# Performance work log

Hardware: AMD Instinct MI355X
Metric: run time of the kernel (lower is better)

## Reference

```python
import jax, jax.numpy as jnp
import numpy as np

N_NODES = 100000
N_EDGES = 3200000
NFEAT, NHID, OPFEAT = 128, 128, 64
EPS = 1e-06


def setup_inputs() -> dict:
    key = jax.random.key(0)
    ks = jax.random.split(key, 20)
    def u(k, shape, s):
        return jax.random.uniform(k, shape, jnp.float32, -s, s)
    inp = {
        'x': jax.random.normal(ks[0], (N_NODES, NFEAT), jnp.float32),
        'edge_rows': jax.random.randint(ks[1], (N_EDGES,), 0, N_NODES, jnp.int32),
        'edge_cols': jax.random.randint(ks[2], (N_EDGES,), 0, N_NODES, jnp.int32),
        'edge_vals': jax.random.uniform(ks[3], (N_EDGES,), jnp.float32),
        # fc layers (torch Linear: weight [out, in])
        'fc1_w': u(ks[4], (NHID, NFEAT), 1.0 / np.sqrt(NFEAT)),
        'fc1_b': u(ks[5], (NHID,), 1.0 / np.sqrt(NFEAT)),
        'fc2_w': u(ks[6], (NHID, NHID), 1.0 / np.sqrt(NHID)),
        'fc2_b': u(ks[7], (NHID,), 1.0 / np.sqrt(NHID)),
        'ln_gamma': jnp.ones((NHID,), jnp.float32),
        'ln_beta': jnp.zeros((NHID,), jnp.float32),
    }
    s = 1.0 / np.sqrt(NHID)
    for i, out_f in zip(range(1, 5), [NHID, NHID, NHID, OPFEAT]):
        k1, k2, k3 = jax.random.split(jax.random.fold_in(key, 100 + i), 3)
        inp[f'gc{i}_wn'] = u(k1, (NHID, out_f), s)
        inp[f'gc{i}_ws'] = u(k2, (NHID, out_f), s)
        inp[f'gc{i}_b'] = u(k3, (out_f,), s)
    return inp


def _gcn_first_order(x, wn, ws, b, rows, cols, vals):
    # act_self + sparse_adj @ (x @ wn) + bias
    act_self = x @ ws                      # [N, out]
    support = x @ wn                       # [N, out]
    gathered = support[cols] * vals[:, None]   # [E, out] irregular gather
    act_neighbor = jax.ops.segment_sum(gathered, rows, num_segments=x.shape[0])
    return act_self + act_neighbor + b


def _layer_norm(x, gamma, beta):
    mean = jnp.mean(x, axis=-1, keepdims=True)
    std = jnp.std(x, axis=-1, keepdims=True, ddof=1)  # torch .std is unbiased
    return gamma * (x - mean) / (std + EPS) + beta


def reference(x, edge_rows, edge_cols, edge_vals,
              fc1_w, fc1_b, fc2_w, fc2_b, ln_gamma, ln_beta,
              gc1_wn, gc1_ws, gc1_b, gc2_wn, gc2_ws, gc2_b,
              gc3_wn, gc3_ws, gc3_b, gc4_wn, gc4_ws, gc4_b):
    h = jax.nn.relu(x @ fc1_w.T + fc1_b)
    h = jax.nn.relu(h @ fc2_w.T + fc2_b)
    h = _layer_norm(h, ln_gamma, ln_beta)
    h = jax.nn.relu(_gcn_first_order(h, gc1_wn, gc1_ws, gc1_b, edge_rows, edge_cols, edge_vals))
    h = jax.nn.relu(_gcn_first_order(h, gc2_wn, gc2_ws, gc2_b, edge_rows, edge_cols, edge_vals))
    h = jax.nn.relu(_gcn_first_order(h, gc3_wn, gc3_ws, gc3_b, edge_rows, edge_cols, edge_vals))
    h = jax.nn.relu(_gcn_first_order(h, gc4_wn, gc4_ws, gc4_b, edge_rows, edge_cols, edge_vals))
    return h
```

## Files before the change

### kernel.cpp

```cpp
#include <hip/hip_runtime.h>

constexpr int N_NODES = 100000;
constexpr int N_EDGES = 3200000;
constexpr float EPS = 1e-6f;

constexpr int NBKT = 196;
constexpr int BKT_SHIFT = 9;
constexpr int BKT_ROWS = 512;
constexpr int ARENA_STRIDE = 18432;
constexpr int EPB1 = 8000;
constexpr int NBLK1 = 400;
constexpr int CAP = 72;

typedef __attribute__((ext_vector_type(8))) short bfrag;
typedef __attribute__((ext_vector_type(4))) float ffrag;

__device__ __forceinline__ unsigned short f2bf(float f) {
    unsigned int u = __float_as_uint(f);
    u += 0x7FFFu + ((u >> 16) & 1u);
    return (unsigned short)(u >> 16);
}
__device__ __forceinline__ float bf_lo(unsigned int w) { return __uint_as_float(w << 16); }
__device__ __forceinline__ float bf_hi(unsigned int w) { return __uint_as_float(w & 0xFFFF0000u); }

__global__ __launch_bounds__(256) void prep_w_k(
    const float* __restrict__ fc1_w, const float* __restrict__ fc2_w,
    const float* __restrict__ wn0, const float* __restrict__ ws0,
    const float* __restrict__ wn1, const float* __restrict__ ws1,
    const float* __restrict__ wn2, const float* __restrict__ ws2,
    const float* __restrict__ wn3, const float* __restrict__ ws3,
    unsigned short* __restrict__ Wb)
{
    int idx = blockIdx.x * 256 + threadIdx.x;
    if (idx >= 147456) return;
    float v;
    if (idx < 32768) {
        int r = idx >> 7, k = idx & 127;
        v = (r < 128) ? fc1_w[r * 128 + k] : fc2_w[(r - 128) * 128 + k];
    } else if (idx < 131072) {
        int idx2 = idx - 32768;
        int l = idx2 >> 15, w = idx2 & 32767;
        int o = w >> 8, k = w & 255;
        const float* wn = l == 0 ? wn0 : l == 1 ? wn1 : wn2;
        const float* ws = l == 0 ? ws0 : l == 1 ? ws1 : ws2;
        v = (k < 128) ? ws[k * 128 + o] : wn[(k - 128) * 128 + o];
    } else {
        int idx3 = idx - 131072;
        int o = idx3 >> 7, k = idx3 & 127;
        v = (o < 64) ? wn3[k * 64 + o] : ws3[k * 64 + (o - 64)];
    }
    Wb[idx] = f2bf(v);
}

template<int MODE, bool A_FP32>
__global__ __launch_bounds__(256, 2) void mfma_gemm_k(
    const void* Av, const unsigned short* __restrict__ Wg_,
    const float* __restrict__ bias,
    const float* __restrict__ gamma, const float* __restrict__ beta,
    unsigned short* __restrict__ Yb, float* Tout)
{
    constexpr int NT = 8;
    __shared__ unsigned short Bs[128 * 136];
    const int tid = threadIdx.x;

    const uint4* Wg = (const uint4*)Wg_;
    uint4* Bs4 = (uint4*)Bs;
    for (int i = tid; i < 128 * 16; i += 256) {
        int n = i >> 4, c = i & 15;
        Bs4[n * 17 + c] = Wg[i];
    }

    const int wave = tid >> 6, lane = tid & 63;
    const int quad = lane >> 4, l16 = lane & 15;
    const long base = (long)blockIdx.x * 128 + wave * 32;

    union AU { uint4 q; bfrag v; unsigned short s[8]; };
    bfrag a[2][4];
#pragma unroll
    for (int mt = 0; mt < 2; mt++) {
        long node = base + mt * 16 + l16;
        bool ok = node < N_NODES;
        if (A_FP32) {
            const float4* Ar = (const float4*)((const float*)Av + node * 128);
#pragma unroll
            for (int t = 0; t < 4; t++) {
                AU u;
                if (ok) {
                    float4 f0 = Ar[t * 8 + quad * 2];
                    float4 f1 = Ar[t * 8 + quad * 2 + 1];
                    u.s[0] = f2bf(f0.x); u.s[1] = f2bf(f0.y);
                    u.s[2] = f2bf(f0.z); u.s[3] = f2bf(f0.w);
                    u.s[4] = f2bf(f1.x); u.s[5] = f2bf(f1.y);
                    u.s[6] = f2bf(f1.z); u.s[7] = f2bf(f1.w);
                } else u.q = make_uint4(0, 0, 0, 0);
                a[mt][t] = u.v;
            }
        } else {
            const uint4* Ar = (const uint4*)((const unsigned short*)Av + node * 128);
#pragma unroll
            for (int t = 0; t < 4; t++) {
                AU u;
                u.q = ok ? Ar[t * 4 + quad] : make_uint4(0, 0, 0, 0);
                a[mt][t] = u.v;
            }
        }
    }
    __syncthreads();

    ffrag acc[2][NT];
#pragma unroll
    for (int mt = 0; mt < 2; mt++)
#pragma unroll
        for (int nt = 0; nt < NT; nt++) acc[mt][nt] = (ffrag)0.f;

#pragma unroll
    for (int t = 0; t < 4; t++)
#pragma unroll
        for (int nt = 0; nt < NT; nt++) {
            bfrag b = *(const bfrag*)&Bs[(nt * 16 + l16) * 136 + t * 32 + quad * 8];
            acc[0][nt] = __builtin_amdgcn_mfma_f32_16x16x32_bf16(a[0][t], b, acc[0][nt], 0, 0, 0);
            acc[1][nt] = __builtin_amdgcn_mfma_f32_16x16x32_bf16(a[1][t], b, acc[1][nt], 0, 0, 0);
        }

    if (MODE == 0) {
        float bv[NT];
#pragma unroll
        for (int nt = 0; nt < NT; nt++) bv[nt] = bias[nt * 16 + l16];
#pragma unroll
        for (int mt = 0; mt < 2; mt++)
#pragma unroll
            for (int reg = 0; reg < 4; reg++) {
                long node = base + mt * 16 + quad * 4 + reg;
                if (node >= N_NODES) continue;
#pragma unroll
                for (int nt = 0; nt < NT; nt++)
                    Yb[node * 128 + nt * 16 + l16] = f2bf(fmaxf(acc[mt][nt][reg] + bv[nt], 0.f));
            }
    } else if (MODE == 1) {
        float bv[NT], gv[NT], bev[NT];
#pragma unroll
        for (int nt = 0; nt < NT; nt++) {
            bv[nt] = bias[nt * 16 + l16];
            gv[nt] = gamma[nt * 16 + l16];
            bev[nt] = beta[nt * 16 + l16];
        }
#pragma unroll
        for (int mt = 0; mt < 2; mt++)
#pragma unroll
            for (int reg = 0; reg < 4; reg++) {
                long node = base + mt * 16 + quad * 4 + reg;
                if (node >= N_NODES) continue;
                float v[NT], s = 0.f, sq = 0.f;
#pragma unroll
                for (int nt = 0; nt < NT; nt++) {
                    v[nt] = fmaxf(acc[mt][nt][reg] + bv[nt], 0.f);
                    s += v[nt]; sq += v[nt] * v[nt];
                }
#pragma unroll
                for (int off = 1; off < 16; off <<= 1) {
                    s  += __shfl_xor(s, off, 64);
                    sq += __shfl_xor(sq, off, 64);
                }
                float mean = s * (1.f / 128.f);
                float var = fmaxf((sq - 128.f * mean * mean) * (1.f / 127.f), 0.f);
                float inv = 1.f / (sqrtf(var) + EPS);
#pragma unroll
                for (int nt = 0; nt < NT; nt++)
                    Yb[node * 128 + nt * 16 + l16] = f2bf(gv[nt] * (v[nt] - mean) * inv + bev[nt]);
            }
    } else {
        float bv[4];
#pragma unroll
        for (int i = 0; i < 4; i++) bv[i] = bias[i * 16 + l16];
#pragma unroll
        for (int mt = 0; mt < 2; mt++)
#pragma unroll
            for (int reg = 0; reg < 4; reg++) {
                long node = base + mt * 16 + quad * 4 + reg;
                if (node >= N_NODES) continue;
#pragma unroll
                for (int nt = 0; nt < 4; nt++)
                    Yb[node * 64 + nt * 16 + l16] = f2bf(acc[mt][nt][reg]);
#pragma unroll
                for (int nt = 4; nt < 8; nt++)
                    Tout[node * 64 + (nt - 4) * 16 + l16] = acc[mt][nt][reg] + bv[nt - 4];
            }
    }
}

__global__ __launch_bounds__(256, 2) void fused_gemm_k(
    const unsigned short* __restrict__ A1, const unsigned short* __restrict__ A2,
    const unsigned short* __restrict__ Wg_, const float* __restrict__ bias,
    unsigned short* __restrict__ Y)
{
    constexpr int NT = 8;
    __shared__ unsigned short Bs[128 * 264];
    const int tid = threadIdx.x;

    const uint4* Wg = (const uint4*)Wg_;
    uint4* Bs4 = (uint4*)Bs;
    for (int i = tid; i < 128 * 32; i += 256) {
        int n = i >> 5, c = i & 31;
        Bs4[n * 33 + c] = Wg[i];
    }

    const int wave = tid >> 6, lane = tid & 63;
    const int quad = lane >> 4, l16 = lane & 15;
    const long base = (long)blockIdx.x * 128 + wave * 32;

    union AU { uint4 q; bfrag v; };
    bfrag a[2][8];
#pragma unroll
    for (int mt = 0; mt < 2; mt++) {
        long node = base + mt * 16 + l16;
        bool ok = node < N_NODES;
        const uint4* A1r = (const uint4*)(A1 + node * 128);
        const uint4* A2r = (const uint4*)(A2 + node * 128);
#pragma unroll
        for (int t = 0; t < 4; t++) {
            AU u1, u2;
            u1.q = ok ? A1r[t * 4 + quad] : make_uint4(0, 0, 0, 0);
            u2.q = ok ? A2r[t * 4 + quad] : make_uint4(0, 0, 0, 0);
            a[mt][t] = u1.v;
            a[mt][4 + t] = u2.v;
        }
    }
    __syncthreads();

    ffrag acc[2][NT];
#pragma unroll
    for (int mt = 0; mt < 2; mt++)
#pragma unroll
        for (int nt = 0; nt < NT; nt++) acc[mt][nt] = (ffrag)0.f;

#pragma unroll
    for (int t = 0; t < 8; t++)
#pragma unroll
        for (int nt = 0; nt < NT; nt++) {
            bfrag b = *(const bfrag*)&Bs[(nt * 16 + l16) * 264 + t * 32 + quad * 8];
            acc[0][nt] = __builtin_amdgcn_mfma_f32_16x16x32_bf16(a[0][t], b, acc[0][nt], 0, 0, 0);
            acc[1][nt] = __builtin_amdgcn_mfma_f32_16x16x32_bf16(a[1][t], b, acc[1][nt], 0, 0, 0);
        }

    float bv[NT];
#pragma unroll
    for (int nt = 0; nt < NT; nt++) bv[nt] = bias[nt * 16 + l16];
#pragma unroll
    for (int mt = 0; mt < 2; mt++)
#pragma unroll
        for (int reg = 0; reg < 4; reg++) {
            long node = base + mt * 16 + quad * 4 + reg;
            if (node >= N_NODES) continue;
#pragma unroll
            for (int nt = 0; nt < NT; nt++)
                Y[node * 128 + nt * 16 + l16] = f2bf(fmaxf(acc[mt][nt][reg] + bv[nt], 0.f));
        }
}

__global__ __launch_bounds__(256) void bin_k(
    const int* __restrict__ rows, const int* __restrict__ cols,
    const float* __restrict__ vals, int* gcur,
    unsigned* __restrict__ arena_e, unsigned short* __restrict__ arena_r)
{
    __shared__ int hist[NBKT];
    __shared__ int lstart[NBKT];
    __shared__ int lcur[NBKT];
    __shared__ int gbase[NBKT];
    __shared__ unsigned st_e[EPB1];
    __shared__ unsigned short st_r[EPB1];
    __shared__ unsigned char st_b[EPB1];
    const int tid = threadIdx.x;
    const int e0 = blockIdx.x * EPB1;
    const int ecnt = min(EPB1, N_EDGES - e0);

    for (int i = tid; i < NBKT; i += 256) hist[i] = 0;
    __syncthreads();
    for (int i = tid; i < ecnt; i += 256)
        atomicAdd(&hist[rows[e0 + i] >> BKT_SHIFT], 1);
    __syncthreads();
    if (tid == 0) {
        int s = 0;
        for (int b = 0; b < NBKT; b++) { lstart[b] = s; s += hist[b]; }
    }
    __syncthreads();
    for (int i = tid; i < NBKT; i += 256) lcur[i] = lstart[i];
    __syncthreads();
    for (int i = tid; i < ecnt; i += 256) {
        int r = rows[e0 + i];
        int b = r >> BKT_SHIFT;
        unsigned entry = ((unsigned)cols[e0 + i] << 15)
                       | (unsigned)(f2bf(vals[e0 + i]) & 0x7FFF);
        int pos = atomicAdd(&lcur[b], 1);
        st_e[pos] = entry;
        st_r[pos] = (unsigned short)(r & (BKT_ROWS - 1));
        st_b[pos] = (unsigned char)b;
    }
    __syncthreads();
    for (int b = tid; b < NBKT; b += 256) {
        int cnt = lcur[b] - lstart[b];
        gbase[b] = cnt > 0 ? atomicAdd(&gcur[b], cnt) : 0;
    }
    __syncthreads();
    for (int i = tid; i < ecnt; i += 256) {
        int b = st_b[i];
        int off = gbase[b] + (i - lstart[b]);
        if (off < ARENA_STRIDE) {
            long dest = (long)b * ARENA_STRIDE + off;
            arena_e[dest] = st_e[i];
            arena_r[dest] = st_r[i];
        }
    }
}

__global__ __launch_bounds__(1024) void build_k(
    const int* __restrict__ gcur, const unsigned* __restrict__ arena_e,
    const unsigned short* __restrict__ arena_r,
    unsigned* __restrict__ csr, int* __restrict__ cursor)
{
    __shared__ int cnt[BKT_ROWS];
    const int tid = threadIdx.x;
    const int b = blockIdx.x;
    for (int i = tid; i < BKT_ROWS; i += 1024) cnt[i] = 0;
    __syncthreads();
    const int ec = min(gcur[b], ARENA_STRIDE);
    const long abase = (long)b * ARENA_STRIDE;
    for (int i = tid; i < ec; i += 1024) {
        unsigned entry = arena_e[abase + i];
        int rib = arena_r[abase + i] & (BKT_ROWS - 1);
        int rank = atomicAdd(&cnt[rib], 1);
        if (rank < CAP)
            csr[((long)b * BKT_ROWS + rib) * CAP + rank] = entry;
    }
    __syncthreads();
    for (int i = tid; i < BKT_ROWS; i += 1024) {
        int gr = b * BKT_ROWS + i;
        if (gr < N_NODES) cursor[gr] = min(cnt[i], CAP);
    }
}

__global__ __launch_bounds__(256) void gather_k(
    const int* __restrict__ cursor, const unsigned* __restrict__ csr,
    const unsigned short* __restrict__ Sb, unsigned short* __restrict__ G)
{
    int node = blockIdx.x * 4 + (threadIdx.x >> 6);
    if (node >= N_NODES) return;
    int lane = threadIdx.x & 63;
    int fl = lane & 15, ep = lane >> 4;
    const long s = (long)node * CAP;
    const int total = min(cursor[node], CAP);

    float acc[8] = {0, 0, 0, 0, 0, 0, 0, 0};
    const uint4* S4 = (const uint4*)Sb;

    for (int base = 0; base < total; base += 64) {
        int idx = base + lane;
        unsigned ed = (idx < total) ? csr[s + idx] : 0u;
        int cnt = total - base; if (cnt > 64) cnt = 64;
        int U = cnt >> 4;
        int j = ep;
        for (int u = 0; u < U; u++, j += 16) {
            unsigned p0 = (unsigned)__shfl((int)ed, j, 64);
            unsigned p1v = (unsigned)__shfl((int)ed, j + 4, 64);
            unsigned p2v = (unsigned)__shfl((int)ed, j + 8, 64);
            unsigned p3v = (unsigned)__shfl((int)ed, j + 12, 64);
            float v0 = __uint_as_float((p0 & 0x7FFFu) << 16);
            float v1 = __uint_as_float((p1v & 0x7FFFu) << 16);
            float v2 = __uint_as_float((p2v & 0x7FFFu) << 16);
            float v3 = __uint_as_float((p3v & 0x7FFFu) << 16);
            uint4 s0 = S4[((p0 >> 15) << 4) + fl];
            uint4 s1 = S4[((p1v >> 15) << 4) + fl];
            uint4 s2 = S4[((p2v >> 15) << 4) + fl];
            uint4 s3 = S4[((p3v >> 15) << 4) + fl];
            acc[0] = fmaf(v0, bf_lo(s0.x), acc[0]); acc[1] = fmaf(v0, bf_hi(s0.x), acc[1]);
            acc[2] = fmaf(v0, bf_lo(s0.y), acc[2]); acc[3] = fmaf(v0, bf_hi(s0.y), acc[3]);
            acc[4] = fmaf(v0, bf_lo(s0.z), acc[4]); acc[5] = fmaf(v0, bf_hi(s0.z), acc[5]);
            acc[6] = fmaf(v0, bf_lo(s0.w), acc[6]); acc[7] = fmaf(v0, bf_hi(s0.w), acc[7]);
            acc[0] = fmaf(v1, bf_lo(s1.x), acc[0]); acc[1] = fmaf(v1, bf_hi(s1.x), acc[1]);
            acc[2] = fmaf(v1, bf_lo(s1.y), acc[2]); acc[3] = fmaf(v1, bf_hi(s1.y), acc[3]);
            acc[4] = fmaf(v1, bf_lo(s1.z), acc[4]); acc[5] = fmaf(v1, bf_hi(s1.z), acc[5]);
            acc[6] = fmaf(v1, bf_lo(s1.w), acc[6]); acc[7] = fmaf(v1, bf_hi(s1.w), acc[7]);
            acc[0] = fmaf(v2, bf_lo(s2.x), acc[0]); acc[1] = fmaf(v2, bf_hi(s2.x), acc[1]);
            acc[2] = fmaf(v2, bf_lo(s2.y), acc[2]); acc[3] = fmaf(v2, bf_hi(s2.y), acc[3]);
            acc[4] = fmaf(v2, bf_lo(s2.z), acc[4]); acc[5] = fmaf(v2, bf_hi(s2.z), acc[5]);
            acc[6] = fmaf(v2, bf_lo(s2.w), acc[6]); acc[7] = fmaf(v2, bf_hi(s2.w), acc[7]);
            acc[0] = fmaf(v3, bf_lo(s3.x), acc[0]); acc[1] = fmaf(v3, bf_hi(s3.x), acc[1]);
            acc[2] = fmaf(v3, bf_lo(s3.y), acc[2]); acc[3] = fmaf(v3, bf_hi(s3.y), acc[3]);
            acc[4] = fmaf(v3, bf_lo(s3.z), acc[4]); acc[5] = fmaf(v3, bf_hi(s3.z), acc[5]);
            acc[6] = fmaf(v3, bf_lo(s3.w), acc[6]); acc[7] = fmaf(v3, bf_hi(s3.w), acc[7]);
        }
        int T = (cnt - (U << 4) + 3) >> 2;
        for (int t = 0; t < T; t++, j += 4) {
            unsigned p0 = (unsigned)__shfl((int)ed, j, 64);
            float v0 = __uint_as_float((p0 & 0x7FFFu) << 16);
            uint4 s0 = S4[((p0 >> 15) << 4) + fl];
            acc[0] = fmaf(v0, bf_lo(s0.x), acc[0]); acc[1] = fmaf(v0, bf_hi(s0.x), acc[1]);
            acc[2] = fmaf(v0, bf_lo(s0.y), acc[2]); acc[3] = fmaf(v0, bf_hi(s0.y), acc[3]);
            acc[4] = fmaf(v0, bf_lo(s0.z), acc[4]); acc[5] = fmaf(v0, bf_hi(s0.z), acc[5]);
            acc[6] = fmaf(v0, bf_lo(s0.w), acc[6]); acc[7] = fmaf(v0, bf_hi(s0.w), acc[7]);
        }
    }
#pragma unroll
    for (int off = 16; off < 64; off <<= 1)
#pragma unroll
        for (int j = 0; j < 8; j++) acc[j] += __shfl_xor(acc[j], off, 64);

    if (ep == 0) {
        uint4 p;
        p.x = (unsigned)f2bf(acc[0]) | ((unsigned)f2bf(acc[1]) << 16);
        p.y = (unsigned)f2bf(acc[2]) | ((unsigned)f2bf(acc[3]) << 16);
        p.z = (unsigned)f2bf(acc[4]) | ((unsigned)f2bf(acc[5]) << 16);
        p.w = (unsigned)f2bf(acc[6]) | ((unsigned)f2bf(acc[7]) << 16);
        ((uint4*)G)[node * 16 + fl] = p;
    }
}

__global__ __launch_bounds__(256) void gather64_k(
    const int* __restrict__ cursor, const unsigned* __restrict__ csr,
    const unsigned short* __restrict__ Sb, const float* __restrict__ T,
    float* __restrict__ out)
{
    int node = blockIdx.x * 4 + (threadIdx.x >> 6);
    if (node >= N_NODES) return;
    int lane = threadIdx.x & 63;
    int fl = lane & 7, ep = lane >> 3;
    const long s = (long)node * CAP;
    const int total = min(cursor[node], CAP);

    float acc[8] = {0, 0, 0, 0, 0, 0, 0, 0};
    const uint4* S4 = (const uint4*)Sb;

    for (int base = 0; base < total; base += 64) {
        int idx = base + lane;
        unsigned ed = (idx < total) ? csr[s + idx] : 0u;
        int cnt = total - base; if (cnt > 64) cnt = 64;
        int U = cnt >> 4;
        int j = ep;
        for (int u = 0; u < U; u++, j += 16) {
            unsigned p0 = (unsigned)__shfl((int)ed, j, 64);
            unsigned p1v = (unsigned)__shfl((int)ed, j + 8, 64);
            float v0 = __uint_as_float((p0 & 0x7FFFu) << 16);
            float v1 = __uint_as_float((p1v & 0x7FFFu) << 16);
            uint4 s0 = S4[((p0 >> 15) << 3) + fl];
            uint4 s1 = S4[((p1v >> 15) << 3) + fl];
            acc[0] = fmaf(v0, bf_lo(s0.x), acc[0]); acc[1] = fmaf(v0, bf_hi(s0.x), acc[1]);
            acc[2] = fmaf(v0, bf_lo(s0.y), acc[2]); acc[3] = fmaf(v0, bf_hi(s0.y), acc[3]);
            acc[4] = fmaf(v0, bf_lo(s0.z), acc[4]); acc[5] = fmaf(v0, bf_hi(s0.z), acc[5]);
            acc[6] = fmaf(v0, bf_lo(s0.w), acc[6]); acc[7] = fmaf(v0, bf_hi(s0.w), acc[7]);
            acc[0] = fmaf(v1, bf_lo(s1.x), acc[0]); acc[1] = fmaf(v1, bf_hi(s1.x), acc[1]);
            acc[2] = fmaf(v1, bf_lo(s1.y), acc[2]); acc[3] = fmaf(v1, bf_hi(s1.y), acc[3]);
            acc[4] = fmaf(v1, bf_lo(s1.z), acc[4]); acc[5] = fmaf(v1, bf_hi(s1.z), acc[5]);
            acc[6] = fmaf(v1, bf_lo(s1.w), acc[6]); acc[7] = fmaf(v1, bf_hi(s1.w), acc[7]);
        }
        int TT = (cnt - (U << 4) + 7) >> 3;
        for (int t = 0; t < TT; t++, j += 8) {
            unsigned p0 = (unsigned)__shfl((int)ed, j, 64);
            float v0 = __uint_as_float((p0 & 0x7FFFu) << 16);
            uint4 s0 = S4[((p0 >> 15) << 3) + fl];
            acc[0] = fmaf(v0, bf_lo(s0.x), acc[0]); acc[1] = fmaf(v0, bf_hi(s0.x), acc[1]);
            acc[2] = fmaf(v0, bf_lo(s0.y), acc[2]); acc[3] = fmaf(v0, bf_hi(s0.y), acc[3]);
            acc[4] = fmaf(v0, bf_lo(s0.z), acc[4]); acc[5] = fmaf(v0, bf_hi(s0.z), acc[5]);
            acc[6] = fmaf(v0, bf_lo(s0.w), acc[6]); acc[7] = fmaf(v0, bf_hi(s0.w), acc[7]);
        }
    }
#pragma unroll
    for (int off = 8; off < 64; off <<= 1)
#pragma unroll
        for (int j = 0; j < 8; j++) acc[j] += __shfl_xor(acc[j], off, 64);

    if (ep == 0) {
        const float4* T4 = (const float4*)T;
        float4 t0 = T4[(long)node * 16 + fl * 2];
        float4 t1 = T4[(long)node * 16 + fl * 2 + 1];
        float4 o0, o1;
        o0.x = fmaxf(acc[0] + t0.x, 0.f); o0.y = fmaxf(acc[1] + t0.y, 0.f);
        o0.z = fmaxf(acc[2] + t0.z, 0.f); o0.w = fmaxf(acc[3] + t0.w, 0.f);
        o1.x = fmaxf(acc[4] + t1.x, 0.f); o1.y = fmaxf(acc[5] + t1.y, 0.f);
        o1.z = fmaxf(acc[6] + t1.z, 0.f); o1.w = fmaxf(acc[7] + t1.w, 0.f);
        ((float4*)out)[(long)node * 16 + fl * 2]     = o0;
        ((float4*)out)[(long)node * 16 + fl * 2 + 1] = o1;
    }
}

extern "C" void kernel_launch(void* const* d_in, const int* in_sizes, int n_in,
                              void* d_out, int out_size, void* d_ws, size_t ws_size,
                              hipStream_t stream)
{
    const float* x     = (const float*)d_in[0];
    const int*   erows = (const int*)d_in[1];
    const int*   ecols = (const int*)d_in[2];
    const float* evals = (const float*)d_in[3];
    const float* fc1_w = (const float*)d_in[4];
    const float* fc1_b = (const float*)d_in[5];
    const float* fc2_w = (const float*)d_in[6];
    const float* fc2_b = (const float*)d_in[7];
    const float* ln_g  = (const float*)d_in[8];
    const float* ln_b  = (const float*)d_in[9];
    const float* gc_wn[4] = {(const float*)d_in[10], (const float*)d_in[13],
                             (const float*)d_in[16], (const float*)d_in[19]};
    const float* gc_ws[4] = {(const float*)d_in[11], (const float*)d_in[14],
                             (const float*)d_in[17], (const float*)d_in[20]};
    const float* gc_b[4]  = {(const float*)d_in[12], (const float*)d_in[15],
                             (const float*)d_in[18], (const float*)d_in[21]};

    unsigned short* Abf = (unsigned short*)d_ws;
    unsigned short* Gbf = Abf + (size_t)N_NODES * 128;
    unsigned* csr = (unsigned*)(Gbf + (size_t)N_NODES * 128);
    unsigned* arena_e = csr + (size_t)N_NODES * CAP;
    unsigned short* arena_r =
        (unsigned short*)(arena_e + (size_t)NBKT * ARENA_STRIDE);
    unsigned short* Wb = arena_r + (size_t)NBKT * ARENA_STRIDE;
    int* cursor = (int*)(Wb + 147456);
    int* gcur   = cursor + N_NODES;
    float* Tf   = (float*)Abf;
    float* out = (float*)d_out;

    dim3 blk(256);
    int gemm_grid = (N_NODES + 127) / 128;
    int node_grid = (N_NODES + 3) / 4;

    hipMemsetAsync(gcur, 0, NBKT * 4, stream);
    bin_k<<<NBLK1, blk, 0, stream>>>(erows, ecols, evals, gcur, arena_e, arena_r);
    build_k<<<NBKT, dim3(1024), 0, stream>>>(gcur, arena_e, arena_r, csr, cursor);

    prep_w_k<<<(147456 + 255) / 256, blk, 0, stream>>>(
        fc1_w, fc2_w, gc_wn[0], gc_ws[0], gc_wn[1], gc_ws[1],
        gc_wn[2], gc_ws[2], gc_wn[3], gc_ws[3], Wb);

    mfma_gemm_k<0, true><<<gemm_grid, blk, 0, stream>>>(
        x, Wb + 0, fc1_b, nullptr, nullptr, Gbf, nullptr);
    mfma_gemm_k<1, false><<<gemm_grid, blk, 0, stream>>>(
        Gbf, Wb + 16384, fc2_b, ln_g, ln_b, Abf, nullptr);

    for (int l = 0; l < 3; l++) {
        gather_k<<<node_grid, blk, 0, stream>>>(cursor, csr, Abf, Gbf);
        fused_gemm_k<<<gemm_grid, blk, 0, stream>>>(
            Abf, Gbf, Wb + 32768 + l * 32768, gc_b[l], Abf);
    }

    mfma_gemm_k<2, false><<<gemm_grid, blk, 0, stream>>>(
        Abf, Wb + 131072, gc_b[3], nullptr, nullptr, Gbf, Tf);
    gather64_k<<<node_grid, blk, 0, stream>>>(cursor, csr, Gbf, Tf, out);
}
```

Before: 709.0 us.

## Fuse neighbor gather with dual-weight GEMM in GCN layers

Merges the per-node sparse gather and the following concatenated GEMM into one kernel. Each block gathers neighbor sums for 128 nodes into a swizzled LDS tile, then runs MFMA against the self and neighbor weights, which it reads straight from global memory. This removes the round trip of the gathered features through global memory and one launch per layer. In exchange the buffers ping-pong, the T buffer gets its own workspace region, and the gather now runs with only 782 blocks of 4 waves, each wave handling 32 nodes in sequence, so there is less parallelism for hiding gather latency.

```diff
diff --git a/kernel.cpp b/kernel.cpp
--- a/kernel.cpp
+++ b/kernel.cpp
@@ -188,75 +188,6 @@
     }
 }
 
-__global__ __launch_bounds__(256, 2) void fused_gemm_k(
-    const unsigned short* __restrict__ A1, const unsigned short* __restrict__ A2,
-    const unsigned short* __restrict__ Wg_, const float* __restrict__ bias,
-    unsigned short* __restrict__ Y)
-{
-    constexpr int NT = 8;
-    __shared__ unsigned short Bs[128 * 264];
-    const int tid = threadIdx.x;
-
-    const uint4* Wg = (const uint4*)Wg_;
-    uint4* Bs4 = (uint4*)Bs;
-    for (int i = tid; i < 128 * 32; i += 256) {
-        int n = i >> 5, c = i & 31;
-        Bs4[n * 33 + c] = Wg[i];
-    }
-
-    const int wave = tid >> 6, lane = tid & 63;
-    const int quad = lane >> 4, l16 = lane & 15;
-    const long base = (long)blockIdx.x * 128 + wave * 32;
-
-    union AU { uint4 q; bfrag v; };
-    bfrag a[2][8];
-#pragma unroll
-    for (int mt = 0; mt < 2; mt++) {
-        long node = base + mt * 16 + l16;
-        bool ok = node < N_NODES;
-        const uint4* A1r = (const uint4*)(A1 + node * 128);
-        const uint4* A2r = (const uint4*)(A2 + node * 128);
-#pragma unroll
-        for (int t = 0; t < 4; t++) {
-            AU u1, u2;
-            u1.q = ok ? A1r[t * 4 + quad] : make_uint4(0, 0, 0, 0);
-            u2.q = ok ? A2r[t * 4 + quad] : make_uint4(0, 0, 0, 0);
-            a[mt][t] = u1.v;
-            a[mt][4 + t] = u2.v;
-        }
-    }
-    __syncthreads();
-
-    ffrag acc[2][NT];
-#pragma unroll
-    for (int mt = 0; mt < 2; mt++)
-#pragma unroll
-        for (int nt = 0; nt < NT; nt++) acc[mt][nt] = (ffrag)0.f;
-
-#pragma unroll
-    for (int t = 0; t < 8; t++)
-#pragma unroll
-        for (int nt = 0; nt < NT; nt++) {
-            bfrag b = *(const bfrag*)&Bs[(nt * 16 + l16) * 264 + t * 32 + quad * 8];
-            acc[0][nt] = __builtin_amdgcn_mfma_f32_16x16x32_bf16(a[0][t], b, acc[0][nt], 0, 0, 0);
-            acc[1][nt] = __builtin_amdgcn_mfma_f32_16x16x32_bf16(a[1][t], b, acc[1][nt], 0, 0, 0);
-        }
-
-    float bv[NT];
-#pragma unroll
-    for (int nt = 0; nt < NT; nt++) bv[nt] = bias[nt * 16 + l16];
-#pragma unroll
-    for (int mt = 0; mt < 2; mt++)
-#pragma unroll
-        for (int reg = 0; reg < 4; reg++) {
-            long node = base + mt * 16 + quad * 4 + reg;
-            if (node >= N_NODES) continue;
-#pragma unroll
-            for (int nt = 0; nt < NT; nt++)
-                Y[node * 128 + nt * 16 + l16] = f2bf(fmaxf(acc[mt][nt][reg] + bv[nt], 0.f));
-        }
-}
-
 __global__ __launch_bounds__(256) void bin_k(
     const int* __restrict__ rows, const int* __restrict__ cols,
     const float* __restrict__ vals, int* gcur,
@@ -338,79 +269,138 @@
     }
 }
 
-__global__ __launch_bounds__(256) void gather_k(
+__global__ __launch_bounds__(256, 4) void gg_k(
     const int* __restrict__ cursor, const unsigned* __restrict__ csr,
-    const unsigned short* __restrict__ Sb, unsigned short* __restrict__ G)
-{
-    int node = blockIdx.x * 4 + (threadIdx.x >> 6);
-    if (node >= N_NODES) return;
-    int lane = threadIdx.x & 63;
-    int fl = lane & 15, ep = lane >> 4;
-    const long s = (long)node * CAP;
-    const int total = min(cursor[node], CAP);
-
-    float acc[8] = {0, 0, 0, 0, 0, 0, 0, 0};
-    const uint4* S4 = (const uint4*)Sb;
-
-    for (int base = 0; base < total; base += 64) {
-        int idx = base + lane;
-        unsigned ed = (idx < total) ? csr[s + idx] : 0u;
-        int cnt = total - base; if (cnt > 64) cnt = 64;
-        int U = cnt >> 4;
-        int j = ep;
-        for (int u = 0; u < U; u++, j += 16) {
-            unsigned p0 = (unsigned)__shfl((int)ed, j, 64);
-            unsigned p1v = (unsigned)__shfl((int)ed, j + 4, 64);
-            unsigned p2v = (unsigned)__shfl((int)ed, j + 8, 64);
-            unsigned p3v = (unsigned)__shfl((int)ed, j + 12, 64);
-            float v0 = __uint_as_float((p0 & 0x7FFFu) << 16);
-            float v1 = __uint_as_float((p1v & 0x7FFFu) << 16);
-            float v2 = __uint_as_float((p2v & 0x7FFFu) << 16);
-            float v3 = __uint_as_float((p3v & 0x7FFFu) << 16);
-            uint4 s0 = S4[((p0 >> 15) << 4) + fl];
-            uint4 s1 = S4[((p1v >> 15) << 4) + fl];
-            uint4 s2 = S4[((p2v >> 15) << 4) + fl];
-            uint4 s3 = S4[((p3v >> 15) << 4) + fl];
-            acc[0] = fmaf(v0, bf_lo(s0.x), acc[0]); acc[1] = fmaf(v0, bf_hi(s0.x), acc[1]);
-            acc[2] = fmaf(v0, bf_lo(s0.y), acc[2]); acc[3] = fmaf(v0, bf_hi(s0.y), acc[3]);
-            acc[4] = fmaf(v0, bf_lo(s0.z), acc[4]); acc[5] = fmaf(v0, bf_hi(s0.z), acc[5]);
-            acc[6] = fmaf(v0, bf_lo(s0.w), acc[6]); acc[7] = fmaf(v0, bf_hi(s0.w), acc[7]);
-            acc[0] = fmaf(v1, bf_lo(s1.x), acc[0]); acc[1] = fmaf(v1, bf_hi(s1.x), acc[1]);
-            acc[2] = fmaf(v1, bf_lo(s1.y), acc[2]); acc[3] = fmaf(v1, bf_hi(s1.y), acc[3]);
-            acc[4] = fmaf(v1, bf_lo(s1.z), acc[4]); acc[5] = fmaf(v1, bf_hi(s1.z), acc[5]);
-            acc[6] = fmaf(v1, bf_lo(s1.w), acc[6]); acc[7] = fmaf(v1, bf_hi(s1.w), acc[7]);
-            acc[0] = fmaf(v2, bf_lo(s2.x), acc[0]); acc[1] = fmaf(v2, bf_hi(s2.x), acc[1]);
-            acc[2] = fmaf(v2, bf_lo(s2.y), acc[2]); acc[3] = fmaf(v2, bf_hi(s2.y), acc[3]);
-            acc[4] = fmaf(v2, bf_lo(s2.z), acc[4]); acc[5] = fmaf(v2, bf_hi(s2.z), acc[5]);
-            acc[6] = fmaf(v2, bf_lo(s2.w), acc[6]); acc[7] = fmaf(v2, bf_hi(s2.w), acc[7]);
-            acc[0] = fmaf(v3, bf_lo(s3.x), acc[0]); acc[1] = fmaf(v3, bf_hi(s3.x), acc[1]);
-            acc[2] = fmaf(v3, bf_lo(s3.y), acc[2]); acc[3] = fmaf(v3, bf_hi(s3.y), acc[3]);
-            acc[4] = fmaf(v3, bf_lo(s3.z), acc[4]); acc[5] = fmaf(v3, bf_hi(s3.z), acc[5]);
-            acc[6] = fmaf(v3, bf_lo(s3.w), acc[6]); acc[7] = fmaf(v3, bf_hi(s3.w), acc[7]);
-        }
-        int T = (cnt - (U << 4) + 3) >> 2;
-        for (int t = 0; t < T; t++, j += 4) {
-            unsigned p0 = (unsigned)__shfl((int)ed, j, 64);
-            float v0 = __uint_as_float((p0 & 0x7FFFu) << 16);
-            uint4 s0 = S4[((p0 >> 15) << 4) + fl];
-            acc[0] = fmaf(v0, bf_lo(s0.x), acc[0]); acc[1] = fmaf(v0, bf_hi(s0.x), acc[1]);
-            acc[2] = fmaf(v0, bf_lo(s0.y), acc[2]); acc[3] = fmaf(v0, bf_hi(s0.y), acc[3]);
-            acc[4] = fmaf(v0, bf_lo(s0.z), acc[4]); acc[5] = fmaf(v0, bf_hi(s0.z), acc[5]);
-            acc[6] = fmaf(v0, bf_lo(s0.w), acc[6]); acc[7] = fmaf(v0, bf_hi(s0.w), acc[7]);
-        }
-    }
-#pragma unroll
-    for (int off = 16; off < 64; off <<= 1)
-#pragma unroll
-        for (int j = 0; j < 8; j++) acc[j] += __shfl_xor(acc[j], off, 64);
-
-    if (ep == 0) {
-        uint4 p;
-        p.x = (unsigned)f2bf(acc[0]) | ((unsigned)f2bf(acc[1]) << 16);
-        p.y = (unsigned)f2bf(acc[2]) | ((unsigned)f2bf(acc[3]) << 16);
-        p.z = (unsigned)f2bf(acc[4]) | ((unsigned)f2bf(acc[5]) << 16);
-        p.w = (unsigned)f2bf(acc[6]) | ((unsigned)f2bf(acc[7]) << 16);
-        ((uint4*)G)[node * 16 + fl] = p;
+    const unsigned short* __restrict__ Ain,
+    const unsigned short* __restrict__ Wg_, const float* __restrict__ bias,
+    unsigned short* __restrict__ Aout)
+{
+    __shared__ unsigned short Gs[128 * 128];
+    const int tid = threadIdx.x;
+    const int wave = tid >> 6, lane = tid & 63;
+    const int fl = lane & 15, ep = lane >> 4;
+    const long blk_base = (long)blockIdx.x * 128;
+    const uint4* S4 = (const uint4*)Ain;
+    uint4* Gs4 = (uint4*)Gs;
+
+    for (int ni = 0; ni < 32; ni++) {
+        const int r = wave * 32 + ni;
+        const long node = blk_base + r;
+        const int total = (node < N_NODES) ? min(cursor[node], CAP) : 0;
+        const long s = node * CAP;
+        float acc[8] = {0, 0, 0, 0, 0, 0, 0, 0};
+
+        for (int base = 0; base < total; base += 64) {
+            int idx = base + lane;
+            unsigned ed = (idx < total) ? csr[s + idx] : 0u;
+            int cnt = total - base; if (cnt > 64) cnt = 64;
+            int U = cnt >> 4;
+            int j = ep;
+            for (int u = 0; u < U; u++, j += 16) {
+                unsigned p0 = (unsigned)__shfl((int)ed, j, 64);
+                unsigned p1v = (unsigned)__shfl((int)ed, j + 4, 64);
+                unsigned p2v = (unsigned)__shfl((int)ed, j + 8, 64);
+                unsigned p3v = (unsigned)__shfl((int)ed, j + 12, 64);
+                float v0 = __uint_as_float((p0 & 0x7FFFu) << 16);
+                float v1 = __uint_as_float((p1v & 0x7FFFu) << 16);
+                float v2 = __uint_as_float((p2v & 0x7FFFu) << 16);
+                float v3 = __uint_as_float((p3v & 0x7FFFu) << 16);
+                uint4 s0 = S4[((p0 >> 15) << 4) + fl];
+                uint4 s1 = S4[((p1v >> 15) << 4) + fl];
+                uint4 s2 = S4[((p2v >> 15) << 4) + fl];
+                uint4 s3 = S4[((p3v >> 15) << 4) + fl];
+                acc[0] = fmaf(v0, bf_lo(s0.x), acc[0]); acc[1] = fmaf(v0, bf_hi(s0.x), acc[1]);
+                acc[2] = fmaf(v0, bf_lo(s0.y), acc[2]); acc[3] = fmaf(v0, bf_hi(s0.y), acc[3]);
+                acc[4] = fmaf(v0, bf_lo(s0.z), acc[4]); acc[5] = fmaf(v0, bf_hi(s0.z), acc[5]);
+                acc[6] = fmaf(v0, bf_lo(s0.w), acc[6]); acc[7] = fmaf(v0, bf_hi(s0.w), acc[7]);
+                acc[0] = fmaf(v1, bf_lo(s1.x), acc[0]); acc[1] = fmaf(v1, bf_hi(s1.x), acc[1]);
+                acc[2] = fmaf(v1, bf_lo(s1.y), acc[2]); acc[3] = fmaf(v1, bf_hi(s1.y), acc[3]);
+                acc[4] = fmaf(v1, bf_lo(s1.z), acc[4]); acc[5] = fmaf(v1, bf_hi(s1.z), acc[5]);
+                acc[6] = fmaf(v1, bf_lo(s1.w), acc[6]); acc[7] = fmaf(v1, bf_hi(s1.w), acc[7]);
+                acc[0] = fmaf(v2, bf_lo(s2.x), acc[0]); acc[1] = fmaf(v2, bf_hi(s2.x), acc[1]);
+                acc[2] = fmaf(v2, bf_lo(s2.y), acc[2]); acc[3] = fmaf(v2, bf_hi(s2.y), acc[3]);
+                acc[4] = fmaf(v2, bf_lo(s2.z), acc[4]); acc[5] = fmaf(v2, bf_hi(s2.z), acc[5]);
+                acc[6] = fmaf(v2, bf_lo(s2.w), acc[6]); acc[7] = fmaf(v2, bf_hi(s2.w), acc[7]);
+                acc[0] = fmaf(v3, bf_lo(s3.x), acc[0]); acc[1] = fmaf(v3, bf_hi(s3.x), acc[1]);
+                acc[2] = fmaf(v3, bf_lo(s3.y), acc[2]); acc[3] = fmaf(v3, bf_hi(s3.y), acc[3]);
+                acc[4] = fmaf(v3, bf_lo(s3.z), acc[4]); acc[5] = fmaf(v3, bf_hi(s3.z), acc[5]);
+                acc[6] = fmaf(v3, bf_lo(s3.w), acc[6]); acc[7] = fmaf(v3, bf_hi(s3.w), acc[7]);
+            }
+            int T = (cnt - (U << 4) + 3) >> 2;
+            for (int t = 0; t < T; t++, j += 4) {
+                unsigned p0 = (unsigned)__shfl((int)ed, j, 64);
+                float v0 = __uint_as_float((p0 & 0x7FFFu) << 16);
+                uint4 s0 = S4[((p0 >> 15) << 4) + fl];
+                acc[0] = fmaf(v0, bf_lo(s0.x), acc[0]); acc[1] = fmaf(v0, bf_hi(s0.x), acc[1]);
+                acc[2] = fmaf(v0, bf_lo(s0.y), acc[2]); acc[3] = fmaf(v0, bf_hi(s0.y), acc[3]);
+                acc[4] = fmaf(v0, bf_lo(s0.z), acc[4]); acc[5] = fmaf(v0, bf_hi(s0.z), acc[5]);
+                acc[6] = fmaf(v0, bf_lo(s0.w), acc[6]); acc[7] = fmaf(v0, bf_hi(s0.w), acc[7]);
+            }
+        }
+#pragma unroll
+        for (int off = 16; off < 64; off <<= 1)
+#pragma unroll
+            for (int j = 0; j < 8; j++) acc[j] += __shfl_xor(acc[j], off, 64);
+
+        if (ep == 0) {
+            uint4 p;
+            p.x = (unsigned)f2bf(acc[0]) | ((unsigned)f2bf(acc[1]) << 16);
+            p.y = (unsigned)f2bf(acc[2]) | ((unsigned)f2bf(acc[3]) << 16);
+            p.z = (unsigned)f2bf(acc[4]) | ((unsigned)f2bf(acc[5]) << 16);
+            p.w = (unsigned)f2bf(acc[6]) | ((unsigned)f2bf(acc[7]) << 16);
+            Gs4[r * 16 + (fl ^ (r & 15))] = p;
+        }
+    }
+    __syncthreads();
+
+    const int quad = ep, l16 = fl;
+    const uint4* Wq = (const uint4*)Wg_;
+    union AU { uint4 q; bfrag v; };
+    float bv[8];
+#pragma unroll
+    for (int nt = 0; nt < 8; nt++) bv[nt] = bias[nt * 16 + l16];
+
+#pragma unroll
+    for (int mt = 0; mt < 2; mt++) {
+        const int gr = wave * 32 + mt * 16 + l16;
+        const long node = blk_base + gr;
+        const bool ok = node < N_NODES;
+        bfrag a1[4], a2[4];
+        const uint4* Ar = (const uint4*)(Ain + node * 128);
+#pragma unroll
+        for (int t = 0; t < 4; t++) {
+            AU u;
+            u.q = ok ? Ar[t * 4 + quad] : make_uint4(0, 0, 0, 0);
+            a1[t] = u.v;
+            AU g;
+            g.q = Gs4[gr * 16 + ((t * 4 + quad) ^ (gr & 15))];
+            a2[t] = g.v;
+        }
+        ffrag acc8[8];
+#pragma unroll
+        for (int nt = 0; nt < 8; nt++) acc8[nt] = (ffrag)0.f;
+#pragma unroll
+        for (int t = 0; t < 4; t++)
+#pragma unroll
+            for (int nt = 0; nt < 8; nt++) {
+                AU b1; b1.q = Wq[(nt * 16 + l16) * 32 + t * 4 + quad];
+                acc8[nt] = __builtin_amdgcn_mfma_f32_16x16x32_bf16(a1[t], b1.v, acc8[nt], 0, 0, 0);
+            }
+#pragma unroll
+        for (int t = 0; t < 4; t++)
+#pragma unroll
+            for (int nt = 0; nt < 8; nt++) {
+                AU b2; b2.q = Wq[(nt * 16 + l16) * 32 + 16 + t * 4 + quad];
+                acc8[nt] = __builtin_amdgcn_mfma_f32_16x16x32_bf16(a2[t], b2.v, acc8[nt], 0, 0, 0);
+            }
+#pragma unroll
+        for (int reg = 0; reg < 4; reg++) {
+            long node2 = blk_base + wave * 32 + mt * 16 + quad * 4 + reg;
+            if (node2 >= N_NODES) continue;
+#pragma unroll
+            for (int nt = 0; nt < 8; nt++)
+                Aout[node2 * 128 + nt * 16 + l16] = f2bf(fmaxf(acc8[nt][reg] + bv[nt], 0.f));
+        }
     }
 }
 
@@ -508,10 +498,10 @@
     unsigned* arena_e = csr + (size_t)N_NODES * CAP;
     unsigned short* arena_r =
         (unsigned short*)(arena_e + (size_t)NBKT * ARENA_STRIDE);
-    unsigned short* Wb = arena_r + (size_t)NBKT * ARENA_STRIDE;
+    float* Tf = (float*)(arena_r + (size_t)NBKT * ARENA_STRIDE);
+    unsigned short* Wb = (unsigned short*)(Tf + (size_t)N_NODES * 64);
     int* cursor = (int*)(Wb + 147456);
     int* gcur   = cursor + N_NODES;
-    float* Tf   = (float*)Abf;
     float* out = (float*)d_out;
 
     dim3 blk(256);
@@ -531,13 +521,11 @@
     mfma_gemm_k<1, false><<<gemm_grid, blk, 0, stream>>>(
         Gbf, Wb + 16384, fc2_b, ln_g, ln_b, Abf, nullptr);
 
-    for (int l = 0; l < 3; l++) {
-        gather_k<<<node_grid, blk, 0, stream>>>(cursor, csr, Abf, Gbf);
-        fused_gemm_k<<<gemm_grid, blk, 0, stream>>>(
-            Abf, Gbf, Wb + 32768 + l * 32768, gc_b[l], Abf);
-    }
+    gg_k<<<gemm_grid, blk, 0, stream>>>(cursor, csr, Abf, Wb + 32768,  gc_b[0], Gbf);
+    gg_k<<<gemm_grid, blk, 0, stream>>>(cursor, csr, Gbf, Wb + 65536,  gc_b[1], Abf);
+    gg_k<<<gemm_grid, blk, 0, stream>>>(cursor, csr, Abf, Wb + 98304,  gc_b[2], Gbf);
 
     mfma_gemm_k<2, false><<<gemm_grid, blk, 0, stream>>>(
-        Abf, Wb + 131072, gc_b[3], nullptr, nullptr, Gbf, Tf);
-    gather64_k<<<node_grid, blk, 0, stream>>>(cursor, csr, Gbf, Tf, out);
-}
+        Gbf, Wb + 131072, gc_b[3], nullptr, nullptr, Abf, Tf);
+    gather64_k<<<node_grid, blk, 0, stream>>>(cursor, csr, Abf, Tf, out);
+}
```

After: 857.9 us. +21.0%, slower.

## Fuse edge binning and first FC GEMM into one heterogeneous kernel launch

Applied to the files above, without the earlier changes.

Merges the edge-binning kernel and the fc1 GEMM into a single launch whose blocks branch on block index, so the independent binning and first GEMM work can run concurrently on the GPU. The fc1 weights are converted to bf16 inside each GEMM block instead of being read from the prepped buffer, and build_k moves after prep_w. This removes a launch and lets the latency-bound binning overlap with the GEMM. The cost is a larger shared allocation per block (59 KB), which may lower occupancy for the GEMM blocks, plus redundant per-block weight conversion.

```diff
diff --git a/kernel.cpp b/kernel.cpp
--- a/kernel.cpp
+++ b/kernel.cpp
@@ -52,7 +52,130 @@
     Wb[idx] = f2bf(v);
 }
 
-template<int MODE, bool A_FP32>
+__global__ __launch_bounds__(256) void front_k(
+    const int* __restrict__ rows, const int* __restrict__ cols,
+    const float* __restrict__ vals, int* gcur,
+    unsigned* __restrict__ arena_e, unsigned short* __restrict__ arena_r,
+    const float* __restrict__ x, const float* __restrict__ fc1_w,
+    const float* __restrict__ fc1_b, unsigned short* __restrict__ Yb)
+{
+    __shared__ __align__(16) char smem[59136];
+    const int tid = threadIdx.x;
+
+    if (blockIdx.x < NBLK1) {
+        int* hist   = (int*)smem;
+        int* lstart = hist + NBKT;
+        int* lcur   = lstart + NBKT;
+        int* gbase  = lcur + NBKT;
+        unsigned* st_e        = (unsigned*)(gbase + NBKT);
+        unsigned short* st_r  = (unsigned short*)(st_e + EPB1);
+        unsigned char* st_b   = (unsigned char*)(st_r + EPB1);
+        const int e0 = blockIdx.x * EPB1;
+        const int ecnt = min(EPB1, N_EDGES - e0);
+
+        for (int i = tid; i < NBKT; i += 256) hist[i] = 0;
+        __syncthreads();
+        for (int i = tid; i < ecnt; i += 256)
+            atomicAdd(&hist[rows[e0 + i] >> BKT_SHIFT], 1);
+        __syncthreads();
+        if (tid == 0) {
+            int s = 0;
+            for (int b = 0; b < NBKT; b++) { lstart[b] = s; s += hist[b]; }
+        }
+        __syncthreads();
+        for (int i = tid; i < NBKT; i += 256) lcur[i] = lstart[i];
+        __syncthreads();
+        for (int i = tid; i < ecnt; i += 256) {
+            int r = rows[e0 + i];
+            int b = r >> BKT_SHIFT;
+            unsigned entry = ((unsigned)cols[e0 + i] << 15)
+                           | (unsigned)(f2bf(vals[e0 + i]) & 0x7FFF);
+            int pos = atomicAdd(&lcur[b], 1);
+            st_e[pos] = entry;
+            st_r[pos] = (unsigned short)(r & (BKT_ROWS - 1));
+            st_b[pos] = (unsigned char)b;
+        }
+        __syncthreads();
+        for (int b = tid; b < NBKT; b += 256) {
+            int cnt = lcur[b] - lstart[b];
+            gbase[b] = cnt > 0 ? atomicAdd(&gcur[b], cnt) : 0;
+        }
+        __syncthreads();
+        for (int i = tid; i < ecnt; i += 256) {
+            int b = st_b[i];
+            int off = gbase[b] + (i - lstart[b]);
+            if (off < ARENA_STRIDE) {
+                long dest = (long)b * ARENA_STRIDE + off;
+                arena_e[dest] = st_e[i];
+                arena_r[dest] = st_r[i];
+            }
+        }
+        return;
+    }
+
+    unsigned short* Bs = (unsigned short*)smem;
+    for (int i = tid; i < 16384; i += 256) {
+        int n = i >> 7, k = i & 127;
+        Bs[n * 136 + k] = f2bf(fc1_w[i]);
+    }
+    const int wave = tid >> 6, lane = tid & 63;
+    const int quad = lane >> 4, l16 = lane & 15;
+    const long base = (long)(blockIdx.x - NBLK1) * 128 + wave * 32;
+
+    union AU { uint4 q; bfrag v; unsigned short s[8]; };
+    bfrag a[2][4];
+#pragma unroll
+    for (int mt = 0; mt < 2; mt++) {
+        long node = base + mt * 16 + l16;
+        bool ok = node < N_NODES;
+        const float4* Ar = (const float4*)(x + node * 128);
+#pragma unroll
+        for (int t = 0; t < 4; t++) {
+            AU u;
+            if (ok) {
+                float4 f0 = Ar[t * 8 + quad * 2];
+                float4 f1 = Ar[t * 8 + quad * 2 + 1];
+                u.s[0] = f2bf(f0.x); u.s[1] = f2bf(f0.y);
+                u.s[2] = f2bf(f0.z); u.s[3] = f2bf(f0.w);
+                u.s[4] = f2bf(f1.x); u.s[5] = f2bf(f1.y);
+                u.s[6] = f2bf(f1.z); u.s[7] = f2bf(f1.w);
+            } else u.q = make_uint4(0, 0, 0, 0);
+            a[mt][t] = u.v;
+        }
+    }
+    __syncthreads();
+
+    ffrag acc[2][8];
+#pragma unroll
+    for (int mt = 0; mt < 2; mt++)
+#pragma unroll
+        for (int nt = 0; nt < 8; nt++) acc[mt][nt] = (ffrag)0.f;
+
+#pragma unroll
+    for (int t = 0; t < 4; t++)
+#pragma unroll
+        for (int nt = 0; nt < 8; nt++) {
+            bfrag b = *(const bfrag*)&Bs[(nt * 16 + l16) * 136 + t * 32 + quad * 8];
+            acc[0][nt] = __builtin_amdgcn_mfma_f32_16x16x32_bf16(a[0][t], b, acc[0][nt], 0, 0, 0);
+            acc[1][nt] = __builtin_amdgcn_mfma_f32_16x16x32_bf16(a[1][t], b, acc[1][nt], 0, 0, 0);
+        }
+
+    float bv[8];
+#pragma unroll
+    for (int nt = 0; nt < 8; nt++) bv[nt] = fc1_b[nt * 16 + l16];
+#pragma unroll
+    for (int mt = 0; mt < 2; mt++)
+#pragma unroll
+        for (int reg = 0; reg < 4; reg++) {
+            long node = base + mt * 16 + quad * 4 + reg;
+            if (node >= N_NODES) continue;
+#pragma unroll
+            for (int nt = 0; nt < 8; nt++)
+                Yb[node * 128 + nt * 16 + l16] = f2bf(fmaxf(acc[mt][nt][reg] + bv[nt], 0.f));
+        }
+}
+
+template<int MODE>
 __global__ __launch_bounds__(256, 2) void mfma_gemm_k(
     const void* Av, const unsigned short* __restrict__ Wg_,
     const float* __restrict__ bias,
@@ -74,35 +197,18 @@
     const int quad = lane >> 4, l16 = lane & 15;
     const long base = (long)blockIdx.x * 128 + wave * 32;
 
-    union AU { uint4 q; bfrag v; unsigned short s[8]; };
+    union AU { uint4 q; bfrag v; };
     bfrag a[2][4];
 #pragma unroll
     for (int mt = 0; mt < 2; mt++) {
         long node = base + mt * 16 + l16;
         bool ok = node < N_NODES;
-        if (A_FP32) {
-            const float4* Ar = (const float4*)((const float*)Av + node * 128);
-#pragma unroll
-            for (int t = 0; t < 4; t++) {
-                AU u;
-                if (ok) {
-                    float4 f0 = Ar[t * 8 + quad * 2];
-                    float4 f1 = Ar[t * 8 + quad * 2 + 1];
-                    u.s[0] = f2bf(f0.x); u.s[1] = f2bf(f0.y);
-                    u.s[2] = f2bf(f0.z); u.s[3] = f2bf(f0.w);
-                    u.s[4] = f2bf(f1.x); u.s[5] = f2bf(f1.y);
-                    u.s[6] = f2bf(f1.z); u.s[7] = f2bf(f1.w);
-                } else u.q = make_uint4(0, 0, 0, 0);
-                a[mt][t] = u.v;
-            }
-        } else {
-            const uint4* Ar = (const uint4*)((const unsigned short*)Av + node * 128);
-#pragma unroll
-            for (int t = 0; t < 4; t++) {
-                AU u;
-                u.q = ok ? Ar[t * 4 + quad] : make_uint4(0, 0, 0, 0);
-                a[mt][t] = u.v;
-            }
+        const uint4* Ar = (const uint4*)((const unsigned short*)Av + node * 128);
+#pragma unroll
+        for (int t = 0; t < 4; t++) {
+            AU u;
+            u.q = ok ? Ar[t * 4 + quad] : make_uint4(0, 0, 0, 0);
+            a[mt][t] = u.v;
         }
     }
     __syncthreads();
@@ -122,21 +228,7 @@
             acc[1][nt] = __builtin_amdgcn_mfma_f32_16x16x32_bf16(a[1][t], b, acc[1][nt], 0, 0, 0);
         }
 
-    if (MODE == 0) {
-        float bv[NT];
-#pragma unroll
-        for (int nt = 0; nt < NT; nt++) bv[nt] = bias[nt * 16 + l16];
-#pragma unroll
-        for (int mt = 0; mt < 2; mt++)
-#pragma unroll
-            for (int reg = 0; reg < 4; reg++) {
-                long node = base + mt * 16 + quad * 4 + reg;
-                if (node >= N_NODES) continue;
-#pragma unroll
-                for (int nt = 0; nt < NT; nt++)
-                    Yb[node * 128 + nt * 16 + l16] = f2bf(fmaxf(acc[mt][nt][reg] + bv[nt], 0.f));
-            }
-    } else if (MODE == 1) {
+    if (MODE == 1) {
         float bv[NT], gv[NT], bev[NT];
 #pragma unroll
         for (int nt = 0; nt < NT; nt++) {
@@ -255,61 +347,6 @@
             for (int nt = 0; nt < NT; nt++)
                 Y[node * 128 + nt * 16 + l16] = f2bf(fmaxf(acc[mt][nt][reg] + bv[nt], 0.f));
         }
-}
-
-__global__ __launch_bounds__(256) void bin_k(
-    const int* __restrict__ rows, const int* __restrict__ cols,
-    const float* __restrict__ vals, int* gcur,
-    unsigned* __restrict__ arena_e, unsigned short* __restrict__ arena_r)
-{
-    __shared__ int hist[NBKT];
-    __shared__ int lstart[NBKT];
-    __shared__ int lcur[NBKT];
-    __shared__ int gbase[NBKT];
-    __shared__ unsigned st_e[EPB1];
-    __shared__ unsigned short st_r[EPB1];
-    __shared__ unsigned char st_b[EPB1];
-    const int tid = threadIdx.x;
-    const int e0 = blockIdx.x * EPB1;
-    const int ecnt = min(EPB1, N_EDGES - e0);
-
-    for (int i = tid; i < NBKT; i += 256) hist[i] = 0;
-    __syncthreads();
-    for (int i = tid; i < ecnt; i += 256)
-        atomicAdd(&hist[rows[e0 + i] >> BKT_SHIFT], 1);
-    __syncthreads();
-    if (tid == 0) {
-        int s = 0;
-        for (int b = 0; b < NBKT; b++) { lstart[b] = s; s += hist[b]; }
-    }
-    __syncthreads();
-    for (int i = tid; i < NBKT; i += 256) lcur[i] = lstart[i];
-    __syncthreads();
-    for (int i = tid; i < ecnt; i += 256) {
-        int r = rows[e0 + i];
-        int b = r >> BKT_SHIFT;
-        unsigned entry = ((unsigned)cols[e0 + i] << 15)
-                       | (unsigned)(f2bf(vals[e0 + i]) & 0x7FFF);
-        int pos = atomicAdd(&lcur[b], 1);
-        st_e[pos] = entry;
-        st_r[pos] = (unsigned short)(r & (BKT_ROWS - 1));
-        st_b[pos] = (unsigned char)b;
-    }
-    __syncthreads();
-    for (int b = tid; b < NBKT; b += 256) {
-        int cnt = lcur[b] - lstart[b];
-        gbase[b] = cnt > 0 ? atomicAdd(&gcur[b], cnt) : 0;
-    }
-    __syncthreads();
-    for (int i = tid; i < ecnt; i += 256) {
-        int b = st_b[i];
-        int off = gbase[b] + (i - lstart[b]);
-        if (off < ARENA_STRIDE) {
-            long dest = (long)b * ARENA_STRIDE + off;
-            arena_e[dest] = st_e[i];
-            arena_r[dest] = st_r[i];
-        }
-    }
 }
 
 __global__ __launch_bounds__(1024) void build_k(
@@ -519,16 +556,17 @@
     int node_grid = (N_NODES + 3) / 4;
 
     hipMemsetAsync(gcur, 0, NBKT * 4, stream);
-    bin_k<<<NBLK1, blk, 0, stream>>>(erows, ecols, evals, gcur, arena_e, arena_r);
-    build_k<<<NBKT, dim3(1024), 0, stream>>>(gcur, arena_e, arena_r, csr, cursor);
+    front_k<<<NBLK1 + gemm_grid, blk, 0, stream>>>(
+        erows, ecols, evals, gcur, arena_e, arena_r,
+        x, fc1_w, fc1_b, Gbf);
 
     prep_w_k<<<(147456 + 255) / 256, blk, 0, stream>>>(
         fc1_w, fc2_w, gc_wn[0], gc_ws[0], gc_wn[1], gc_ws[1],
         gc_wn[2], gc_ws[2], gc_wn[3], gc_ws[3], Wb);
 
-    mfma_gemm_k<0, true><<<gemm_grid, blk, 0, stream>>>(
-        x, Wb + 0, fc1_b, nullptr, nullptr, Gbf, nullptr);
-    mfma_gemm_k<1, false><<<gemm_grid, blk, 0, stream>>>(
+    build_k<<<NBKT, dim3(1024), 0, stream>>>(gcur, arena_e, arena_r, csr, cursor);
+
+    mfma_gemm_k<1><<<gemm_grid, blk, 0, stream>>>(
         Gbf, Wb + 16384, fc2_b, ln_g, ln_b, Abf, nullptr);
 
     for (int l = 0; l < 3; l++) {
@@ -537,7 +575,7 @@
             Abf, Gbf, Wb + 32768 + l * 32768, gc_b[l], Abf);
     }
 
-    mfma_gemm_k<2, false><<<gemm_grid, blk, 0, stream>>>(
+    mfma_gemm_k<2><<<gemm_grid, blk, 0, stream>>>(
         Abf, Wb + 131072, gc_b[3], nullptr, nullptr, Gbf, Tf);
     gather64_k<<<node_grid, blk, 0, stream>>>(cursor, csr, Gbf, Tf, out);
 }
```

Result: no change. 705.7 us (-0.5%).
